# Performance work log

Measured on AMD Instinct MI355X. Metric: run time of the kernel, lower is better.

The kernel has to match this reference:

```python
import jax, jax.numpy as jnp
import numpy as np

DIM = 256
HEADS = 4
DIM_HEAD = 32
HIDDEN = HEADS * DIM_HEAD  # 128
EPS = 1e-5


def setup_inputs() -> dict:
    key = jax.random.key(0)
    ks = jax.random.split(key, 6)
    B, H, W = 16, 64, 64
    x = jax.random.normal(ks[0], (B, DIM, H, W), dtype=jnp.float32)
    # 1x1 conv weights stored as [out_ch, in_ch]
    W_qkv = jax.random.normal(ks[1], (HIDDEN * 3, DIM), dtype=jnp.float32) * 0.02
    W_out = jax.random.normal(ks[2], (DIM, HIDDEN), dtype=jnp.float32) * 0.02
    b_out = jnp.zeros((DIM,), dtype=jnp.float32)
    gamma = jnp.ones((DIM,), dtype=jnp.float32)
    beta = jnp.zeros((DIM,), dtype=jnp.float32)
    return {"x": x, "W_qkv": W_qkv, "W_out": W_out, "b_out": b_out,
            "gamma": gamma, "beta": beta}


def reference(x, W_qkv, W_out, b_out, gamma, beta):
    b, c, h, w = x.shape
    n = h * w
    scale = DIM_HEAD ** -0.5
    # 1x1 conv == channel matmul
    qkv = jnp.einsum('bchw,oc->bohw', x, W_qkv)  # [b, 3*hidden, h, w]
    q, k, v = jnp.split(qkv, 3, axis=1)
    def to_heads(t):
        return t.reshape(b, HEADS, DIM_HEAD, n)  # b h d n
    q = jax.nn.softmax(to_heads(q), axis=-2) * scale  # softmax over d
    k = jax.nn.softmax(to_heads(k), axis=-1)           # softmax over n
    v = to_heads(v)
    # context: [b, h, d, e] — tiny 32x32 per head
    context = jnp.einsum('bhdn,bhen->bhde', k, v)
    out = jnp.einsum('bhde,bhdn->bhen', context, q)  # [b, h, e, n]
    out = out.reshape(b, HIDDEN, h, w)
    # output 1x1 conv with bias
    out = jnp.einsum('bchw,oc->bohw', out, W_out) + b_out[None, :, None, None]
    # GroupNorm(1, dim): normalize over (C,H,W) per sample, per-channel affine
    mean = out.mean(axis=(1, 2, 3), keepdims=True)
    var = out.var(axis=(1, 2, 3), keepdims=True)
    out = (out - mean) * jax.lax.rsqrt(var + EPS)
    return out * gamma[None, :, None, None] + beta[None, :, None, None]
```

## Files before the change

kernel.cpp:

```cpp
#include <hip/hip_runtime.h>

#define NN 4096
#define CIN 256
#define O3 384
#define HID 128
#define NHEAD 4
#define DH 32

typedef float f32x4 __attribute__((ext_vector_type(4)));
typedef _Float16 f16x8 __attribute__((ext_vector_type(8)));
typedef _Float16 f16x4 __attribute__((ext_vector_type(4)));
typedef _Float16 f16x2 __attribute__((ext_vector_type(2)));
typedef __fp16 fp16x2_raw __attribute__((ext_vector_type(2)));

__device__ __forceinline__ f16x2 pkrtz(float a, float b) {
  fp16x2_raw r = __builtin_amdgcn_cvt_pkrtz(a, b);
  return __builtin_bit_cast(f16x2, r);
}

__global__ __launch_bounds__(256) void prep(
    const float* __restrict__ Wqkv, const float* __restrict__ Wout,
    _Float16* __restrict__ WpkA, _Float16* __restrict__ WpkB,
    float* __restrict__ zbase, int nz) {
  const int bid = blockIdx.x, tid = threadIdx.x;
  if (bid < 48) {
    int t = bid * 256 + tid;
    int l = t & 63, mk = t >> 6;
    int k32 = mk & 7, m16 = mk >> 3;
    int row = m16 * 16 + (l & 15), k = k32 * 32 + (l >> 4) * 8;
    const float* s = Wqkv + (size_t)row * CIN + k;
    f16x8 o;
#pragma unroll
    for (int j = 0; j < 8; j++) o[j] = (_Float16)s[j];
    *(f16x8*)(WpkA + (size_t)t * 8) = o;
  } else if (bid < 64) {
    int t = (bid - 48) * 256 + tid;
    int l = t & 63, mk = t >> 6;
    int k32 = mk & 3, m16 = mk >> 2;
    int row = m16 * 16 + (l & 15), k = k32 * 32 + (l >> 4) * 8;
    const float* s = Wout + (size_t)row * HID + k;
    f16x8 o;
#pragma unroll
    for (int j = 0; j < 8; j++) o[j] = (_Float16)s[j];
    *(f16x8*)(WpkB + (size_t)t * 8) = o;
  } else {
    int i = (bid - 64) * 256 + tid;
    if (i < nz) zbase[i] = 0.f;
  }
}

__global__ __launch_bounds__(256) void gemm_qkv(
    const float* __restrict__ X, const _Float16* __restrict__ Wpk,
    _Float16* __restrict__ Yt) {
  __shared__ _Float16 Bs[2][128 * 40];
  const int orig = blockIdx.x;
  const int swz = (orig & 7) * 192 + (orig >> 3);
  const int mt = swz % 3;
  const int nb = swz / 3;
  const int n0 = (nb & 31) << 7;
  const int b  = nb >> 5;
  const float* Xb = X + (size_t)b * CIN * NN;
  _Float16* Yb = Yt + (size_t)b * NN * O3;
  const int tid = threadIdx.x, l = tid & 63, wid = tid >> 6;
  const int wm = (wid >> 1) << 6, wn = (wid & 1) << 6;
  const int fr = l & 15, q = l >> 4;
  const int b_n = (tid & 31) << 2, b_kk = (tid >> 5) << 2;
  const int am16 = mt * 8 + (wm >> 4);
  const int tp = tid & 31;
  const int swz3 = ((tp ^ (tp >> 2)) & 3) << 1;
  const int gw4 = (((tid >> 5) ^ swz3) << 2);
  int roff[4];
#pragma unroll
  for (int fn = 0; fn < 4; fn++) {
    const int R = wn + fn * 16 + fr;
    const int sR = ((R >> 2) ^ (R >> 4)) & 3;
    roff[fn] = R * 40 + ((q ^ sR) << 3);
  }

#define LOADX(dst, t_) do { \
    _Pragma("unroll") \
    for (int r_ = 0; r_ < 4; r_++) \
      dst[r_] = *(const f32x4*)(Xb + (size_t)((t_) * 32 + b_kk + r_) * NN + n0 + b_n); \
  } while (0)
#define LOADAH(dst, t_) do { \
    _Pragma("unroll") \
    for (int fm_ = 0; fm_ < 4; fm_++) \
      dst[fm_] = *(const f16x8*)(Wpk + ((size_t)((am16 + fm_) * 8 + (t_)) * 64 + l) * 8); \
  } while (0)
#define CVTW(buf_, src) do { \
    _Pragma("unroll") \
    for (int j_ = 0; j_ < 4; j_++) { \
      f16x2 p0_ = pkrtz(src[0][j_], src[1][j_]); \
      f16x2 p1_ = pkrtz(src[2][j_], src[3][j_]); \
      *(f16x4*)&Bs[buf_][(b_n + j_) * 40 + gw4] = (f16x4){p0_[0], p0_[1], p1_[0], p1_[1]}; \
    } } while (0)

  f32x4 xr[2][4];
  f16x8 ah[2][4];
  f32x4 acc[4][4];
#pragma unroll
  for (int i = 0; i < 4; i++)
#pragma unroll
    for (int j = 0; j < 4; j++) acc[i][j] = (f32x4){0.f, 0.f, 0.f, 0.f};

  LOADX(xr[0], 0);
  CVTW(0, xr[0]);
  LOADAH(ah[0], 0);
  LOADX(xr[1], 1);
  asm volatile("s_waitcnt lgkmcnt(0)" ::: "memory");
  __builtin_amdgcn_s_barrier();
  __builtin_amdgcn_sched_barrier(0);

#pragma unroll
  for (int t = 0; t < 8; t++) {
    const int cur = t & 1, nxt = cur ^ 1;
    f16x8 bh[4];
#pragma unroll
    for (int fn = 0; fn < 4; fn++)
      bh[fn] = *(const f16x8*)&Bs[cur][roff[fn]];
#pragma unroll
    for (int fm = 0; fm < 4; fm++)
#pragma unroll
      for (int fn = 0; fn < 4; fn++)
        acc[fm][fn] = __builtin_amdgcn_mfma_f32_16x16x32_f16(ah[cur][fm], bh[fn], acc[fm][fn], 0, 0, 0);
    if (t < 7) {
      CVTW(nxt, xr[nxt]);
      LOADAH(ah[nxt], t + 1);
      if (t < 6) LOADX(xr[cur], t + 2);
    }
    asm volatile("s_waitcnt lgkmcnt(0)" ::: "memory");
    __builtin_amdgcn_s_barrier();
    __builtin_amdgcn_sched_barrier(0);
  }

#pragma unroll
  for (int fm = 0; fm < 4; fm++) {
    int mrow = mt * 128 + wm + fm * 16 + q * 4;
#pragma unroll
    for (int fn = 0; fn < 4; fn++) {
      int n = n0 + wn + fn * 16 + fr;
      f16x2 h0 = pkrtz(acc[fm][fn][0], acc[fm][fn][1]);
      f16x2 h1 = pkrtz(acc[fm][fn][2], acc[fm][fn][3]);
      *(f16x4*)(Yb + (size_t)n * O3 + mrow) = (f16x4){h0[0], h0[1], h1[0], h1[1]};
    }
  }
#undef LOADX
#undef LOADAH
#undef CVTW
}

__global__ __launch_bounds__(256) void attn1(
    const _Float16* __restrict__ qkvt, float* __restrict__ ctx_raw,
    float* __restrict__ srow_raw) {
  const int h = blockIdx.x, b = blockIdx.y, ns = blockIdx.z;
  const _Float16* base = qkvt + (size_t)b * NN * O3;
  const _Float16* Kb = base + HID + h * DH;
  const _Float16* Vb = base + 2 * HID + h * DH;
  float* ctx = ctx_raw + (size_t)(b * NHEAD + h) * (DH * DH);
  float* srow = srow_raw + (size_t)(b * NHEAD + h) * DH;
  __shared__ __align__(16) float Es[64][36];
  __shared__ __align__(16) float Vs[64][36];
  __shared__ float ctxs[DH][DH + 1];
  __shared__ float srow_s[DH];
  const int tid = threadIdx.x, l = tid & 63, w = tid >> 6;
  const int d4 = (l >> 3) << 2, e4 = (l & 7) << 2;
  if (tid < DH) srow_s[tid] = 0.f;
  for (int i = tid; i < DH * (DH + 1); i += 256) (&ctxs[0][0])[i] = 0.f;
  float sacc[4] = {0.f, 0.f, 0.f, 0.f};
  float acc[4][4];
#pragma unroll
  for (int i = 0; i < 4; i++)
#pragma unroll
    for (int j = 0; j < 4; j++) acc[i][j] = 0.f;

  for (int c = 0; c < 8; c++) {
    const int n0 = ns * 512 + c * 64;
    const size_t roff = (size_t)(n0 + l) * O3 + w * 8;
    f16x8 kv = *(const f16x8*)(Kb + roff);
    f16x8 vv = *(const f16x8*)(Vb + roff);
    __syncthreads();
    float4 e0, e1, v0, v1;
    e0.x = __expf((float)kv[0]); e0.y = __expf((float)kv[1]);
    e0.z = __expf((float)kv[2]); e0.w = __expf((float)kv[3]);
    e1.x = __expf((float)kv[4]); e1.y = __expf((float)kv[5]);
    e1.z = __expf((float)kv[6]); e1.w = __expf((float)kv[7]);
    v0.x = (float)vv[0]; v0.y = (float)vv[1]; v0.z = (float)vv[2]; v0.w = (float)vv[3];
    v1.x = (float)vv[4]; v1.y = (float)vv[5]; v1.z = (float)vv[6]; v1.w = (float)vv[7];
    *(float4*)&Es[l][w * 8] = e0;
    *(float4*)&Es[l][w * 8 + 4] = e1;
    *(float4*)&Vs[l][w * 8] = v0;
    *(float4*)&Vs[l][w * 8 + 4] = v1;
    __syncthreads();
#pragma unroll
    for (int it = 0; it < 16; it++) {
      const int n = w + 4 * it;
      float ka[4], va[4];
      *(float4*)ka = *(const float4*)&Es[n][d4];
      *(float4*)va = *(const float4*)&Vs[n][e4];
#pragma unroll
      for (int i = 0; i < 4; i++) {
        sacc[i] += ka[i];
#pragma unroll
        for (int j = 0; j < 4; j++) acc[i][j] = fmaf(ka[i], va[j], acc[i][j]);
      }
    }
  }
  if ((l & 7) == 0) {
#pragma unroll
    for (int i = 0; i < 4; i++) atomicAdd(&srow_s[d4 + i], sacc[i]);
  }
#pragma unroll
  for (int i = 0; i < 4; i++)
#pragma unroll
    for (int j = 0; j < 4; j++) atomicAdd(&ctxs[d4 + i][e4 + j], acc[i][j]);
  __syncthreads();
  for (int i = tid; i < DH * DH; i += 256) atomicAdd(&ctx[i], ctxs[i >> 5][i & 31]);
  if (tid < DH) atomicAdd(&srow[tid], srow_s[tid]);
}

__global__ __launch_bounds__(256) void attn2(
    _Float16* __restrict__ qkvt, const float* __restrict__ ctx_raw,
    const float* __restrict__ srow_raw) {
  const int ns = blockIdx.x, h = blockIdx.y, b = blockIdx.z;
  const float* cg = ctx_raw + (size_t)(b * NHEAD + h) * (DH * DH);
  const float* sr = srow_raw + (size_t)(b * NHEAD + h) * DH;
  __shared__ float ctxs[DH][DH + 1];
  const int tid = threadIdx.x;
  for (int i = tid; i < DH * DH; i += 256) ctxs[i >> 5][i & 31] = cg[i] / sr[i >> 5];
  __syncthreads();
  const int n = ns * 256 + tid;
  _Float16* qp = qkvt + ((size_t)b * NN + n) * O3 + h * DH;
  float qv[DH];
#pragma unroll
  for (int i = 0; i < 4; i++) {
    f16x8 v = *(const f16x8*)(qp + i * 8);
#pragma unroll
    for (int j = 0; j < 8; j++) qv[i * 8 + j] = (float)v[j];
  }
  float m = -1e30f;
#pragma unroll
  for (int d = 0; d < DH; d++) m = fmaxf(m, qv[d]);
  float s = 0.f;
#pragma unroll
  for (int d = 0; d < DH; d++) { qv[d] = __expf(qv[d] - m); s += qv[d]; }
  float inv = 0.17677669529663687f / s;
#pragma unroll
  for (int d = 0; d < DH; d++) qv[d] *= inv;
#pragma unroll
  for (int eo = 0; eo < 4; eo++) {
    float o[8];
#pragma unroll
    for (int j = 0; j < 8; j++) o[j] = 0.f;
#pragma unroll
    for (int d = 0; d < DH; d++) {
      float qd = qv[d];
#pragma unroll
      for (int j = 0; j < 8; j++) o[j] = fmaf(ctxs[d][eo * 8 + j], qd, o[j]);
    }
    f16x2 h0 = pkrtz(o[0], o[1]);
    f16x2 h1 = pkrtz(o[2], o[3]);
    f16x2 h2 = pkrtz(o[4], o[5]);
    f16x2 h3 = pkrtz(o[6], o[7]);
    f16x8 ov = (f16x8){h0[0], h0[1], h1[0], h1[1], h2[0], h2[1], h3[0], h3[1]};
    *(f16x8*)(qp + eo * 8) = ov;
  }
}

__global__ __launch_bounds__(256) void gemm_proj(
    const _Float16* __restrict__ At, const _Float16* __restrict__ Wpk,
    const float* __restrict__ bias, float* __restrict__ out,
    double* __restrict__ stats) {
  __shared__ _Float16 Bs[128][40];
  const int mt = blockIdx.x;
  const int n0 = blockIdx.y * 128;
  const int b = blockIdx.z;
  const _Float16* Ab = At + (size_t)b * NN * O3;
  float* outb = out + (size_t)b * CIN * NN;
  const int tid = threadIdx.x, l = tid & 63, wid = tid >> 6;
  const int wm = (wid >> 1) << 6, wn = (wid & 1) << 6;
  const int fr = l & 15, q = l >> 4, kq = q << 3;
  const int am16 = mt * 8 + (wm >> 4);
  const int sr0 = tid >> 2, sc = (tid & 3) << 3;

  f32x4 acc[4][4];
#pragma unroll
  for (int i = 0; i < 4; i++)
#pragma unroll
    for (int j = 0; j < 4; j++) acc[i][j] = (f32x4){0.f, 0.f, 0.f, 0.f};

  for (int k0 = 0; k0 < HID; k0 += 32) {
    f16x8 v0 = *(const f16x8*)(Ab + (size_t)(n0 + sr0) * O3 + k0 + sc);
    f16x8 v1 = *(const f16x8*)(Ab + (size_t)(n0 + 64 + sr0) * O3 + k0 + sc);
    f16x8 ah[4];
#pragma unroll
    for (int fm = 0; fm < 4; fm++)
      ah[fm] = *(const f16x8*)(Wpk + ((size_t)((am16 + fm) * 4 + (k0 >> 5)) * 64 + l) * 8);
    __syncthreads();
    *(f16x8*)&Bs[sr0][sc] = v0;
    *(f16x8*)&Bs[64 + sr0][sc] = v1;
    __syncthreads();
    f16x8 bh[4];
#pragma unroll
    for (int fn = 0; fn < 4; fn++)
      bh[fn] = *(const f16x8*)&Bs[wn + fn * 16 + fr][kq];
#pragma unroll
    for (int fm = 0; fm < 4; fm++)
#pragma unroll
      for (int fn = 0; fn < 4; fn++)
        acc[fm][fn] = __builtin_amdgcn_mfma_f32_16x16x32_f16(ah[fm], bh[fn], acc[fm][fn], 0, 0, 0);
  }
  float lsum = 0.f, lsq = 0.f;
#pragma unroll
  for (int fm = 0; fm < 4; fm++) {
    int rowb = mt * 128 + wm + fm * 16 + q * 4;
#pragma unroll
    for (int r = 0; r < 4; r++) {
      float bv = bias[rowb + r];
      float* dst = outb + (size_t)(rowb + r) * NN + n0 + wn + fr;
#pragma unroll
      for (int fn = 0; fn < 4; fn++) {
        float v = acc[fm][fn][r] + bv;
        dst[fn * 16] = v;
        lsum += v;
        lsq += v * v;
      }
    }
  }
  double ds = (double)lsum, dq = (double)lsq;
#pragma unroll
  for (int off = 32; off; off >>= 1) {
    ds += __shfl_down(ds, off);
    dq += __shfl_down(dq, off);
  }
  __shared__ double sred[8];
  if (l == 0) { sred[wid] = ds; sred[4 + wid] = dq; }
  __syncthreads();
  if (tid == 0) {
    atomicAdd(&stats[b * 2 + 0], sred[0] + sred[1] + sred[2] + sred[3]);
    atomicAdd(&stats[b * 2 + 1], sred[4] + sred[5] + sred[6] + sred[7]);
  }
}

__global__ __launch_bounds__(256) void gn_norm(
    float* __restrict__ out, const double* __restrict__ stats,
    const float* __restrict__ gamma, const float* __restrict__ beta) {
  const int b = blockIdx.y;
  const double nels = (double)CIN * (double)NN;
  double S = stats[b * 2 + 0], Q2 = stats[b * 2 + 1];
  double mu = S / nels;
  double var = Q2 / nels - mu * mu;
  float mean = (float)mu;
  float rstd = (float)rsqrt(var + 1e-5);
  size_t i4 = (size_t)blockIdx.x * 256 + threadIdx.x;
  int c = (int)((i4 * 4) >> 12);
  float g = gamma[c] * rstd, bt = beta[c];
  float4* p = (float4*)(out + (size_t)b * CIN * NN) + i4;
  float4 v = *p;
  v.x = (v.x - mean) * g + bt;
  v.y = (v.y - mean) * g + bt;
  v.z = (v.z - mean) * g + bt;
  v.w = (v.w - mean) * g + bt;
  *p = v;
}

extern "C" void kernel_launch(void* const* d_in, const int* in_sizes, int n_in,
                              void* d_out, int out_size, void* d_ws, size_t ws_size,
                              hipStream_t stream) {
  const float* x     = (const float*)d_in[0];
  const float* Wqkv  = (const float*)d_in[1];
  const float* Wout  = (const float*)d_in[2];
  const float* bout  = (const float*)d_in[3];
  const float* gamma = (const float*)d_in[4];
  const float* beta  = (const float*)d_in[5];
  float* out = (float*)d_out;

  char* ws = (char*)d_ws;
  _Float16* qkvt = (_Float16*)ws;
  size_t off = (size_t)16 * NN * O3 * 2;
  _Float16* WpkA = (_Float16*)(ws + off); off += 48 * 256 * 8 * 2;
  _Float16* WpkB = (_Float16*)(ws + off); off += 16 * 256 * 8 * 2;
  float* ctxg = (float*)(ws + off); off += (size_t)16 * NHEAD * DH * DH * 4;
  float* srow = (float*)(ws + off); off += (size_t)16 * NHEAD * DH * 4;
  double* stats = (double*)(ws + off);

  const int nz = 16 * NHEAD * DH * DH + 16 * NHEAD * DH + 64;
  prep<<<64 + (nz + 255) / 256, 256, 0, stream>>>(Wqkv, Wout, WpkA, WpkB, ctxg, nz);
  gemm_qkv<<<dim3(1536), 256, 0, stream>>>(x, WpkA, qkvt);
  attn1<<<dim3(NHEAD, 16, 8), 256, 0, stream>>>(qkvt, ctxg, srow);
  attn2<<<dim3(16, NHEAD, 16), 256, 0, stream>>>(qkvt, ctxg, srow);
  gemm_proj<<<dim3(2, 32, 16), 256, 0, stream>>>(qkvt, WpkB, bout, out, stats);
  gn_norm<<<dim3(1024, 16), 256, 0, stream>>>(out, stats, gamma, beta);
}
```

Baseline: 130.4 us.

## Recompute output projection twice to fuse GroupNorm and avoid output round-trip

Splits the output projection into a stats-only pass that computes the GEMM and accumulates GroupNorm sums without storing anything, and a second pass that recomputes the GEMM and writes the normalized result directly. This drops the separate normalization kernel, which had to read and rewrite the full fp32 output, in exchange for doing the small K=128 projection GEMM twice. The output is 64 MB of fp32, so skipping one read and one write of it is meant to outweigh the extra MFMA work and the extra fp16 input reads.

```diff
diff --git a/kernel.cpp b/kernel.cpp
--- a/kernel.cpp
+++ b/kernel.cpp
@@ -266,10 +266,82 @@
   }
 }
 
-__global__ __launch_bounds__(256) void gemm_proj(
+__global__ __launch_bounds__(256) void proj_stats(
+    const _Float16* __restrict__ At, const _Float16* __restrict__ Wpk,
+    const float* __restrict__ bias, double* __restrict__ stats) {
+  __shared__ _Float16 Bs[128][40];
+  const int mt = blockIdx.x;
+  const int n0 = blockIdx.y * 128;
+  const int b = blockIdx.z;
+  const _Float16* Ab = At + (size_t)b * NN * O3;
+  const int tid = threadIdx.x, l = tid & 63, wid = tid >> 6;
+  const int wm = (wid >> 1) << 6, wn = (wid & 1) << 6;
+  const int fr = l & 15, q = l >> 4, kq = q << 3;
+  const int am16 = mt * 8 + (wm >> 4);
+  const int sr0 = tid >> 2, sc = (tid & 3) << 3;
+
+  f32x4 acc[4][4];
+#pragma unroll
+  for (int i = 0; i < 4; i++)
+#pragma unroll
+    for (int j = 0; j < 4; j++) acc[i][j] = (f32x4){0.f, 0.f, 0.f, 0.f};
+
+  for (int k0 = 0; k0 < HID; k0 += 32) {
+    f16x8 v0 = *(const f16x8*)(Ab + (size_t)(n0 + sr0) * O3 + k0 + sc);
+    f16x8 v1 = *(const f16x8*)(Ab + (size_t)(n0 + 64 + sr0) * O3 + k0 + sc);
+    f16x8 ah[4];
+#pragma unroll
+    for (int fm = 0; fm < 4; fm++)
+      ah[fm] = *(const f16x8*)(Wpk + ((size_t)((am16 + fm) * 4 + (k0 >> 5)) * 64 + l) * 8);
+    __syncthreads();
+    *(f16x8*)&Bs[sr0][sc] = v0;
+    *(f16x8*)&Bs[64 + sr0][sc] = v1;
+    __syncthreads();
+    f16x8 bh[4];
+#pragma unroll
+    for (int fn = 0; fn < 4; fn++)
+      bh[fn] = *(const f16x8*)&Bs[wn + fn * 16 + fr][kq];
+#pragma unroll
+    for (int fm = 0; fm < 4; fm++)
+#pragma unroll
+      for (int fn = 0; fn < 4; fn++)
+        acc[fm][fn] = __builtin_amdgcn_mfma_f32_16x16x32_f16(ah[fm], bh[fn], acc[fm][fn], 0, 0, 0);
+  }
+  float lsum = 0.f, lsq = 0.f;
+#pragma unroll
+  for (int fm = 0; fm < 4; fm++) {
+    int rowb = mt * 128 + wm + fm * 16 + q * 4;
+#pragma unroll
+    for (int r = 0; r < 4; r++) {
+      float bv = bias[rowb + r];
+#pragma unroll
+      for (int fn = 0; fn < 4; fn++) {
+        float v = acc[fm][fn][r] + bv;
+        lsum += v;
+        lsq += v * v;
+      }
+    }
+  }
+  double ds = (double)lsum, dq = (double)lsq;
+#pragma unroll
+  for (int off = 32; off; off >>= 1) {
+    ds += __shfl_down(ds, off);
+    dq += __shfl_down(dq, off);
+  }
+  __shared__ double sred[8];
+  if (l == 0) { sred[wid] = ds; sred[4 + wid] = dq; }
+  __syncthreads();
+  if (tid == 0) {
+    atomicAdd(&stats[b * 2 + 0], sred[0] + sred[1] + sred[2] + sred[3]);
+    atomicAdd(&stats[b * 2 + 1], sred[4] + sred[5] + sred[6] + sred[7]);
+  }
+}
+
+__global__ __launch_bounds__(256) void proj_write(
     const _Float16* __restrict__ At, const _Float16* __restrict__ Wpk,
     const float* __restrict__ bias, float* __restrict__ out,
-    double* __restrict__ stats) {
+    const double* __restrict__ stats, const float* __restrict__ gamma,
+    const float* __restrict__ beta) {
   __shared__ _Float16 Bs[128][40];
   const int mt = blockIdx.x;
   const int n0 = blockIdx.y * 128;
@@ -282,6 +354,13 @@
   const int am16 = mt * 8 + (wm >> 4);
   const int sr0 = tid >> 2, sc = (tid & 3) << 3;
 
+  const double nels = (double)CIN * (double)NN;
+  double S = stats[b * 2 + 0], Q2 = stats[b * 2 + 1];
+  double mu = S / nels;
+  double var = Q2 / nels - mu * mu;
+  const float mean = (float)mu;
+  const float rstd = (float)rsqrt(var + 1e-5);
+
   f32x4 acc[4][4];
 #pragma unroll
   for (int i = 0; i < 4; i++)
@@ -309,58 +388,22 @@
       for (int fn = 0; fn < 4; fn++)
         acc[fm][fn] = __builtin_amdgcn_mfma_f32_16x16x32_f16(ah[fm], bh[fn], acc[fm][fn], 0, 0, 0);
   }
-  float lsum = 0.f, lsq = 0.f;
 #pragma unroll
   for (int fm = 0; fm < 4; fm++) {
     int rowb = mt * 128 + wm + fm * 16 + q * 4;
 #pragma unroll
     for (int r = 0; r < 4; r++) {
-      float bv = bias[rowb + r];
-      float* dst = outb + (size_t)(rowb + r) * NN + n0 + wn + fr;
+      int row = rowb + r;
+      float bv = bias[row];
+      float g = gamma[row] * rstd, bt = beta[row];
+      float* dst = outb + (size_t)row * NN + n0 + wn + fr;
 #pragma unroll
       for (int fn = 0; fn < 4; fn++) {
         float v = acc[fm][fn][r] + bv;
-        dst[fn * 16] = v;
-        lsum += v;
-        lsq += v * v;
+        dst[fn * 16] = (v - mean) * g + bt;
       }
     }
   }
-  double ds = (double)lsum, dq = (double)lsq;
-#pragma unroll
-  for (int off = 32; off; off >>= 1) {
-    ds += __shfl_down(ds, off);
-    dq += __shfl_down(dq, off);
-  }
-  __shared__ double sred[8];
-  if (l == 0) { sred[wid] = ds; sred[4 + wid] = dq; }
-  __syncthreads();
-  if (tid == 0) {
-    atomicAdd(&stats[b * 2 + 0], sred[0] + sred[1] + sred[2] + sred[3]);
-    atomicAdd(&stats[b * 2 + 1], sred[4] + sred[5] + sred[6] + sred[7]);
-  }
-}
-
-__global__ __launch_bounds__(256) void gn_norm(
-    float* __restrict__ out, const double* __restrict__ stats,
-    const float* __restrict__ gamma, const float* __restrict__ beta) {
-  const int b = blockIdx.y;
-  const double nels = (double)CIN * (double)NN;
-  double S = stats[b * 2 + 0], Q2 = stats[b * 2 + 1];
-  double mu = S / nels;
-  double var = Q2 / nels - mu * mu;
-  float mean = (float)mu;
-  float rstd = (float)rsqrt(var + 1e-5);
-  size_t i4 = (size_t)blockIdx.x * 256 + threadIdx.x;
-  int c = (int)((i4 * 4) >> 12);
-  float g = gamma[c] * rstd, bt = beta[c];
-  float4* p = (float4*)(out + (size_t)b * CIN * NN) + i4;
-  float4 v = *p;
-  v.x = (v.x - mean) * g + bt;
-  v.y = (v.y - mean) * g + bt;
-  v.z = (v.z - mean) * g + bt;
-  v.w = (v.w - mean) * g + bt;
-  *p = v;
 }
 
 extern "C" void kernel_launch(void* const* d_in, const int* in_sizes, int n_in,
@@ -388,6 +431,6 @@
   gemm_qkv<<<dim3(1536), 256, 0, stream>>>(x, WpkA, qkvt);
   attn1<<<dim3(NHEAD, 16, 8), 256, 0, stream>>>(qkvt, ctxg, srow);
   attn2<<<dim3(16, NHEAD, 16), 256, 0, stream>>>(qkvt, ctxg, srow);
-  gemm_proj<<<dim3(2, 32, 16), 256, 0, stream>>>(qkvt, WpkB, bout, out, stats);
-  gn_norm<<<dim3(1024, 16), 256, 0, stream>>>(out, stats, gamma, beta);
-}
+  proj_stats<<<dim3(2, 32, 16), 256, 0, stream>>>(qkvt, WpkB, bout, stats);
+  proj_write<<<dim3(2, 32, 16), 256, 0, stream>>>(qkvt, WpkB, bout, out, stats, gamma, beta);
+}
```

After: 123.8 us. 1.05x faster.
